# Performance work log

Hardware: AMD Instinct MI355X
Metric: run time of the kernel (lower is better)

The kernel has to match this reference:

```python
import jax, jax.numpy as jnp
import numpy as np

N_FUNS = 10  # subset of SYMBOLIC_LIB safe on all of R

def _apply_funs(z, fun_ids):
    # z: (batch, out, in); fun_ids: (out, in) int ids selecting the symbolic fn
    branches = [
        z,                      # 0: 'x'
        z * z,                  # 1: 'x^2'
        z * z * z,              # 2: 'x^3'
        jnp.sin(z),             # 3: 'sin'
        jnp.tanh(z),            # 4: 'tanh'
        jax.nn.sigmoid(z),      # 5: 'sigmoid'
        jnp.exp(-z * z),        # 6: 'gaussian'
        jnp.abs(z),             # 7: 'abs'
        jnp.arctan(z),          # 8: 'arctan'
        jnp.exp(z),             # 9: 'exp'
    ]
    ids = fun_ids[None, :, :]  # broadcast over batch
    return jnp.select([ids == k for k in range(N_FUNS)], branches)


def setup_inputs() -> dict:
    key = jax.random.key(0)
    k1, k2, k3 = jax.random.split(key, 3)
    batch, in_f, out_f = 4096, 128, 128
    x = jax.random.normal(k1, (batch, in_f), dtype=jnp.float32)
    affine = jax.random.normal(k2, (out_f, in_f, 4), dtype=jnp.float32)
    mask = jnp.eye(in_f, dtype=jnp.float32)  # default buffer: identity
    fun_ids = jax.random.randint(k3, (out_f, in_f), 0, N_FUNS, dtype=jnp.int32)
    return {"x": x, "affine": affine, "mask": mask, "fun_ids": fun_ids}


def reference(x, affine, mask, fun_ids):
    # reduce inputs through the mask (identity by default): (batch, reduced_in)
    x_red = jnp.einsum("bi,ri->br", x, mask)
    a = affine[None, :, :, 0]  # (1, out, in)
    b = affine[None, :, :, 1]
    c = affine[None, :, :, 2]
    d = affine[None, :, :, 3]
    z = a * x_red[:, None, :] + b          # (batch, out, in)
    postacts = c * _apply_funs(z, fun_ids) + d  # (batch, out, in)
    y = jnp.sum(postacts, axis=2)           # (batch, out)
    return y, postacts
```

## Files before the change

### kernel.cpp

```cpp
#include <hip/hip_runtime.h>
#include <cmath>

#define XR_RT   32
#define XR_BC   32
#define OGROUP  8
#define BCHUNK  16

typedef float nfloat4 __attribute__((ext_vector_type(4)));

__global__ __launch_bounds__(256) void xred_kernel(const float* __restrict__ x,
                                                   const float* __restrict__ mask,
                                                   float* __restrict__ xred) {
    __shared__ float ms[XR_RT][129];
    __shared__ float xs[128][40];
    const int tid = threadIdx.x;
    const int r0  = blockIdx.x * XR_RT;
    const int b0  = blockIdx.y * XR_BC;

    const float4* m4 = (const float4*)(mask + (size_t)r0 * 128);
    for (int k = tid; k < XR_RT * 32; k += 256) {
        float4 v = m4[k];
        int row = k >> 5;
        int col = (k & 31) * 4;
        ms[row][col]     = v.x;
        ms[row][col + 1] = v.y;
        ms[row][col + 2] = v.z;
        ms[row][col + 3] = v.w;
    }
    for (int k = tid; k < XR_BC * 128; k += 256) {
        int b = k >> 7, i = k & 127;
        xs[i][b] = x[(size_t)(b0 + b) * 128 + i];
    }
    __syncthreads();

    const int r = tid & 31;
    const int g = tid >> 5;
    float acc[4] = {0.f, 0.f, 0.f, 0.f};
    for (int i = 0; i < 128; ++i) {
        const float  m  = ms[r][i];
        const float4 xa = *(const float4*)&xs[i][4 * g];
        acc[0] += m * xa.x; acc[1] += m * xa.y; acc[2] += m * xa.z; acc[3] += m * xa.w;
    }
    #pragma unroll
    for (int j = 0; j < 4; ++j)
        xred[(size_t)(b0 + 4 * g + j) * 128 + (r0 + r)] = acc[j];
}

__global__ __launch_bounds__(256) void kan_main(const float4* __restrict__ xred4,
                                                const float4* __restrict__ affine,
                                                const int* __restrict__ fun_ids,
                                                float* __restrict__ y,
                                                float4* __restrict__ post4) {
    const int tid = threadIdx.x;
    const int oo  = tid >> 5;
    const int il  = tid & 31;
    const int o   = blockIdx.x * OGROUP + oo;

    float4 A[4]; int f[4];
    #pragma unroll
    for (int j = 0; j < 4; ++j) {
        A[j] = affine[(size_t)o * 128 + il * 4 + j];
        f[j] = fun_ids[(size_t)o * 128 + il * 4 + j];
    }

    bool m1[4], m2[4], m3[4], m7[4], m8[4], me[4];
    float k1[4], k2[4], An[4], Bn[4], Dd[4];
    #pragma unroll
    for (int j = 0; j < 4; ++j) {
        const int fj = f[j];
        m1[j] = (fj == 1); m2[j] = (fj == 2); m3[j] = (fj == 3);
        m7[j] = (fj == 7); m8[j] = (fj == 8);
        me[j] = (fj >= 4 && fj <= 6) || (fj == 9);
        float k1v = 0.f, k2v = 0.f, Anv = 0.f, Bnv = 1.f, Ddv = 0.f;
        if      (fj == 4) { k1v = -2.f; Anv = 1.f; Bnv = -1.f; Ddv = 1.f; }
        else if (fj == 5) { k1v = -1.f; Anv = 1.f; Bnv =  0.f; Ddv = 1.f; }
        else if (fj == 6) { k2v = -1.f; }
        else if (fj == 9) { k1v =  1.f; }
        k1[j] = k1v; k2[j] = k2v; An[j] = Anv; Bn[j] = Bnv; Dd[j] = Ddv;
    }

    const int b0 = blockIdx.y * BCHUNK;

    float4 xr = xred4[(size_t)b0 * 32 + il];

    #pragma unroll 2
    for (int bb = 0; bb < BCHUNK; ++bb) {
        const int b = b0 + bb;
        float4 xr_n = xr;
        if (bb + 1 < BCHUNK) xr_n = xred4[(size_t)(b + 1) * 32 + il];

        const float xv[4] = {xr.x, xr.y, xr.z, xr.w};

        float p[4];
        #pragma unroll
        for (int j = 0; j < 4; ++j) {
            const float z  = fmaf(A[j].x, xv[j], A[j].y);
            const float zz = z * z;
            float pv = m1[j] ? zz : z;
            pv = m2[j] ? zz * z : pv;
            pv = m7[j] ? fabsf(z) : pv;
            const float s = __sinf(z);
            pv = m3[j] ? s : pv;
            const float arg = fminf(fmaf(k2[j], zz, k1[j] * z), 80.f);
            const float e   = __expf(arg);
            const float num = fmaf(Bn[j], e, An[j]);
            const float den = fmaf(Dd[j], e, 1.0f);
            const float r   = num * __builtin_amdgcn_rcpf(den);
            pv = me[j] ? r : pv;
            const float az  = fabsf(z);
            const bool  big = az > 1.0f;
            const float t   = big ? __builtin_amdgcn_rcpf(az) : az;
            const float t2  = t * t;
            float q = fmaf(t2, 0.079331f, -0.288679f);
            q = fmaf(t2, q, 0.995354f);
            q = t * q;
            q = big ? 1.57079632679f - q : q;
            const float at = copysignf(q, z);
            pv = m8[j] ? at : pv;
            p[j] = fmaf(A[j].z, pv, A[j].w);
        }

        nfloat4 pv4 = {p[0], p[1], p[2], p[3]};
        __builtin_nontemporal_store(pv4,
            reinterpret_cast<nfloat4*>(&post4[((size_t)b * 128 + o) * 32 + il]));

        float s = (p[0] + p[1]) + (p[2] + p[3]);
        s += __shfl_xor(s, 1, 64);
        s += __shfl_xor(s, 2, 64);
        s += __shfl_xor(s, 4, 64);
        s += __shfl_xor(s, 8, 64);
        s += __shfl_xor(s, 16, 64);
        if (il == 0) __builtin_nontemporal_store(s, &y[(size_t)b * 128 + o]);

        xr = xr_n;
    }
}

extern "C" void kernel_launch(void* const* d_in, const int* in_sizes, int n_in,
                              void* d_out, int out_size, void* d_ws, size_t ws_size,
                              hipStream_t stream) {
    const float* x       = (const float*)d_in[0];
    const float* affine  = (const float*)d_in[1];
    const float* mask    = (const float*)d_in[2];
    const int*   fun_ids = (const int*)d_in[3];

    const int batch = in_sizes[0] / 128;

    float* xred     = (float*)d_ws;
    float* y        = (float*)d_out;
    float* postacts = y + (size_t)batch * 128;

    xred_kernel<<<dim3(128 / XR_RT, batch / XR_BC), dim3(256), 0, stream>>>(x, mask, xred);

    kan_main<<<dim3(128 / OGROUP, batch / BCHUNK), dim3(256), 0, stream>>>(
        (const float4*)xred, (const float4*)affine, fun_ids, y, (float4*)postacts);
}
```

Baseline: 306.3 us.

## Sort edges by function class per block to cut wavefront divergence

Each block now bins its 1024 (out,in) edges into five function classes with a shared-memory histogram and counting sort. Threads then handle class-homogeneous edges, so each wavefront mostly runs one branch instead of evaluating sin, exp and arctan for every element. Results are scattered back through a double-buffered shared array to keep postacts stores coalesced. This adds per-block sort overhead, gathered xred loads, a barrier per batch row, and a higher-degree arctan polynomial.

New measurement: 318.4 us. +4.0%, slower.

```diff
diff --git a/kernel.cpp b/kernel.cpp
--- a/kernel.cpp
+++ b/kernel.cpp
@@ -5,6 +5,7 @@
 #define XR_BC   32
 #define OGROUP  8
 #define BCHUNK  16
+#define NSLOT   (OGROUP * 128)
 
 typedef float nfloat4 __attribute__((ext_vector_type(4)));
 
@@ -46,85 +47,133 @@
         xred[(size_t)(b0 + 4 * g + j) * 128 + (r0 + r)] = acc[j];
 }
 
-__global__ __launch_bounds__(256) void kan_main(const float4* __restrict__ xred4,
+__global__ __launch_bounds__(256) void kan_main(const float* __restrict__ xred,
                                                 const float4* __restrict__ affine,
                                                 const int* __restrict__ fun_ids,
                                                 float* __restrict__ y,
                                                 float4* __restrict__ post4) {
+    __shared__ int hist[8];
+    __shared__ int base[8];
+    __shared__ unsigned short sorted[NSLOT];
+    __shared__ float pbuf[2][NSLOT];
+
     const int tid = threadIdx.x;
+    const int reg = blockIdx.x;
+    const int b0  = blockIdx.y * BCHUNK;
     const int oo  = tid >> 5;
     const int il  = tid & 31;
-    const int o   = blockIdx.x * OGROUP + oo;
-
-    float4 A[4]; int f[4];
+    const int o   = reg * OGROUP + oo;
+
+    if (tid < 8) hist[tid] = 0;
+    __syncthreads();
+
+    const int4 fid = ((const int4*)(fun_ids + (size_t)reg * NSLOT))[tid];
+    const int myid[4] = {fid.x, fid.y, fid.z, fid.w};
+    int mycls[4];
     #pragma unroll
     for (int j = 0; j < 4; ++j) {
-        A[j] = affine[(size_t)o * 128 + il * 4 + j];
-        f[j] = fun_ids[(size_t)o * 128 + il * 4 + j];
-    }
-
-    bool m1[4], m2[4], m3[4], m7[4], m8[4], me[4];
-    float k1[4], k2[4], An[4], Bn[4], Dd[4];
+        const int id = myid[j];
+        mycls[j] = (id == 3) ? 1 : (id == 4 || id == 5) ? 2
+                 : (id == 6 || id == 9) ? 3 : (id == 8) ? 4 : 0;
+        atomicAdd(&hist[mycls[j]], 1);
+    }
+    __syncthreads();
+    if (tid == 0) {
+        int acc = 0;
+        #pragma unroll
+        for (int c = 0; c < 5; ++c) { base[c] = acc; acc += hist[c]; }
+    }
+    __syncthreads();
     #pragma unroll
     for (int j = 0; j < 4; ++j) {
-        const int fj = f[j];
-        m1[j] = (fj == 1); m2[j] = (fj == 2); m3[j] = (fj == 3);
-        m7[j] = (fj == 7); m8[j] = (fj == 8);
-        me[j] = (fj >= 4 && fj <= 6) || (fj == 9);
-        float k1v = 0.f, k2v = 0.f, Anv = 0.f, Bnv = 1.f, Ddv = 0.f;
-        if      (fj == 4) { k1v = -2.f; Anv = 1.f; Bnv = -1.f; Ddv = 1.f; }
-        else if (fj == 5) { k1v = -1.f; Anv = 1.f; Bnv =  0.f; Ddv = 1.f; }
-        else if (fj == 6) { k2v = -1.f; }
-        else if (fj == 9) { k1v =  1.f; }
-        k1[j] = k1v; k2[j] = k2v; An[j] = Anv; Bn[j] = Bnv; Dd[j] = Ddv;
-    }
-
-    const int b0 = blockIdx.y * BCHUNK;
-
-    float4 xr = xred4[(size_t)b0 * 32 + il];
-
-    #pragma unroll 2
+        const int pos = atomicAdd(&base[mycls[j]], 1);
+        sorted[pos] = (unsigned short)((4 * tid + j) | (myid[j] << 10));
+    }
+    __syncthreads();
+
+    int   slt[4], ii[4], cls[4];
+    float Aa[4], Ab[4], Ac[4], Ad[4];
+    bool  m1[4], m2[4], m7[4];
+    float k1[4], k2[4], An[4], Bn[4];
+    #pragma unroll
+    for (int j = 0; j < 4; ++j) {
+        const int v  = sorted[4 * tid + j];
+        const int sl = v & 1023;
+        const int id = v >> 10;
+        slt[j] = sl;
+        ii[j]  = sl & 127;
+        cls[j] = (id == 3) ? 1 : (id == 4 || id == 5) ? 2
+               : (id == 6 || id == 9) ? 3 : (id == 8) ? 4 : 0;
+        const float4 A = affine[(size_t)reg * NSLOT + sl];
+        Aa[j] = A.x; Ab[j] = A.y; Ac[j] = A.z; Ad[j] = A.w;
+        m1[j] = (id == 1); m2[j] = (id == 2); m7[j] = (id == 7);
+        float k1v = 0.f, k2v = 0.f, Anv = 0.f, Bnv = 1.f;
+        if      (id == 4) { k1v = -2.f; Anv = 1.f; Bnv = -1.f; }
+        else if (id == 5) { k1v = -1.f; Anv = 1.f; Bnv =  0.f; }
+        else if (id == 6) { k2v = -1.f; }
+        else if (id == 9) { k1v =  1.f; }
+        k1[j] = k1v; k2[j] = k2v; An[j] = Anv; Bn[j] = Bnv;
+    }
+
+    float xg[4];
+    #pragma unroll
+    for (int j = 0; j < 4; ++j) xg[j] = xred[(size_t)b0 * 128 + ii[j]];
+
+    int par = 0;
     for (int bb = 0; bb < BCHUNK; ++bb) {
         const int b = b0 + bb;
-        float4 xr_n = xr;
-        if (bb + 1 < BCHUNK) xr_n = xred4[(size_t)(b + 1) * 32 + il];
-
-        const float xv[4] = {xr.x, xr.y, xr.z, xr.w};
+        float xn[4] = {xg[0], xg[1], xg[2], xg[3]};
+        if (bb + 1 < BCHUNK) {
+            #pragma unroll
+            for (int j = 0; j < 4; ++j) xn[j] = xred[(size_t)(b + 1) * 128 + ii[j]];
+        }
 
         float p[4];
         #pragma unroll
         for (int j = 0; j < 4; ++j) {
-            const float z  = fmaf(A[j].x, xv[j], A[j].y);
-            const float zz = z * z;
-            float pv = m1[j] ? zz : z;
-            pv = m2[j] ? zz * z : pv;
-            pv = m7[j] ? fabsf(z) : pv;
-            const float s = __sinf(z);
-            pv = m3[j] ? s : pv;
-            const float arg = fminf(fmaf(k2[j], zz, k1[j] * z), 80.f);
-            const float e   = __expf(arg);
-            const float num = fmaf(Bn[j], e, An[j]);
-            const float den = fmaf(Dd[j], e, 1.0f);
-            const float r   = num * __builtin_amdgcn_rcpf(den);
-            pv = me[j] ? r : pv;
-            const float az  = fabsf(z);
-            const bool  big = az > 1.0f;
-            const float t   = big ? __builtin_amdgcn_rcpf(az) : az;
-            const float t2  = t * t;
-            float q = fmaf(t2, 0.079331f, -0.288679f);
-            q = fmaf(t2, q, 0.995354f);
-            q = t * q;
-            q = big ? 1.57079632679f - q : q;
-            const float at = copysignf(q, z);
-            pv = m8[j] ? at : pv;
-            p[j] = fmaf(A[j].z, pv, A[j].w);
+            const float z = fmaf(Aa[j], xg[j], Ab[j]);
+            float pv;
+            const int cj = cls[j];
+            if (cj == 0) {
+                const float zz = z * z;
+                pv = m1[j] ? zz : z;
+                pv = m2[j] ? zz * z : pv;
+                pv = m7[j] ? fabsf(z) : pv;
+            } else if (cj == 1) {
+                pv = __sinf(z);
+            } else if (cj == 2) {
+                const float e = __expf(fminf(k1[j] * z, 80.f));
+                pv = fmaf(Bn[j], e, An[j]) * __builtin_amdgcn_rcpf(1.f + e);
+            } else if (cj == 3) {
+                const float arg = fminf(fmaf(k2[j], z * z, k1[j] * z), 80.f);
+                pv = __expf(arg);
+            } else {
+                const float az  = fabsf(z);
+                const bool  big = az > 1.0f;
+                const float t   = big ? __builtin_amdgcn_rcpf(az) : az;
+                const float t2  = t * t;
+                float q = fmaf(t2, -0.01172120f, 0.05265332f);
+                q = fmaf(t2, q, -0.11643287f);
+                q = fmaf(t2, q,  0.19354346f);
+                q = fmaf(t2, q, -0.33262347f);
+                q = fmaf(t2, q,  0.99997726f);
+                q = t * q;
+                q = big ? 1.57079632679f - q : q;
+                pv = copysignf(q, z);
+            }
+            p[j] = fmaf(Ac[j], pv, Ad[j]);
         }
 
-        nfloat4 pv4 = {p[0], p[1], p[2], p[3]};
-        __builtin_nontemporal_store(pv4,
+        #pragma unroll
+        for (int j = 0; j < 4; ++j) pbuf[par][slt[j]] = p[j];
+        __syncthreads();
+
+        const float4 q = *(const float4*)&pbuf[par][4 * tid];
+        nfloat4 outv = {q.x, q.y, q.z, q.w};
+        __builtin_nontemporal_store(outv,
             reinterpret_cast<nfloat4*>(&post4[((size_t)b * 128 + o) * 32 + il]));
 
-        float s = (p[0] + p[1]) + (p[2] + p[3]);
+        float s = (q.x + q.y) + (q.z + q.w);
         s += __shfl_xor(s, 1, 64);
         s += __shfl_xor(s, 2, 64);
         s += __shfl_xor(s, 4, 64);
@@ -132,7 +181,9 @@
         s += __shfl_xor(s, 16, 64);
         if (il == 0) __builtin_nontemporal_store(s, &y[(size_t)b * 128 + o]);
 
-        xr = xr_n;
+        par ^= 1;
+        #pragma unroll
+        for (int j = 0; j < 4; ++j) xg[j] = xn[j];
     }
 }
 
@@ -153,5 +204,5 @@
     xred_kernel<<<dim3(128 / XR_RT, batch / XR_BC), dim3(256), 0, stream>>>(x, mask, xred);
 
     kan_main<<<dim3(128 / OGROUP, batch / BCHUNK), dim3(256), 0, stream>>>(
-        (const float4*)xred, (const float4*)affine, fun_ids, y, (float4*)postacts);
+        xred, (const float4*)affine, fun_ids, y, (float4*)postacts);
 }
```
